# Performance work log

Hardware: AMD Instinct MI355X
Metric: run time of the kernel (lower is better)

Reference implementation:

```python
import jax, jax.numpy as jnp
import numpy as np

C, H, W = 8, 8, 8
A = 6            # action_dim
LATENT = 64
HID = 64
GRU_IN = HID + A + LATENT  # 134


def _conv(x, w):
    return jax.lax.conv_general_dilated(
        x, w, (1, 1), 'VALID', dimension_numbers=('NCHW', 'OIHW', 'NCHW'))


def setup_inputs() -> dict:
    key = jax.random.key(0)
    ks = jax.random.split(key, 20)
    B, N, T = 64, 10, 128
    s_h = jax.random.normal(ks[0], (B, N, T, C, H, W), jnp.float32)
    a_h = jax.random.randint(ks[1], (B, N, T), 0, A).astype(jnp.int64)
    b_z = jax.random.normal(ks[2], (B, LATENT), jnp.float32)
    s = 0.05
    p = {
        'conv1_w': jax.random.normal(ks[3], (32, C, 3, 3)) * s,
        'conv1_b': jnp.zeros((32,)),
        'conv2_w': jax.random.normal(ks[4], (32, 32, 3, 3)) * s,
        'conv2_b': jnp.zeros((32,)),
        'fc_w': jax.random.normal(ks[5], (HID, 32 * 4 * 4)) * s,
        'fc_b': jnp.zeros((HID,)),
        'emb': jax.random.normal(ks[6], (A, A)) * s,
        'gru_wih': jax.random.normal(ks[7], (3 * HID, GRU_IN)) * s,
        'gru_whh': jax.random.normal(ks[8], (3 * HID, HID)) * s,
        'gru_bih': jnp.zeros((3 * HID,)),
        'gru_bhh': jnp.zeros((3 * HID,)),
        'mlp1_w': jax.random.normal(ks[9], (HID, HID)) * s,
        'mlp1_b': jnp.zeros((HID,)),
        'mlp2_w': jax.random.normal(ks[10], (A, HID)) * s,
        'mlp2_b': jnp.zeros((A,)),
    }
    return {'s_h': s_h, 'a_h': a_h, 'b_z': b_z, **p}


def reference(s_h, a_h, b_z, conv1_w, conv1_b, conv2_w, conv2_b, fc_w, fc_b,
              emb, gru_wih, gru_whh, gru_bih, gru_bhh,
              mlp1_w, mlp1_b, mlp2_w, mlp2_b):
    B, N = s_h.shape[0], s_h.shape[1]
    T = a_h.shape[2]
    BN = B * N

    # action mask, [B, N, T, 1]
    action_masks = (a_h != A - 1)[..., None].astype(jnp.float32)

    # --- state encoder on first frame only ---
    s0 = s_h[:, :, 0].reshape(BN, C, H, W)
    x = jax.nn.relu(_conv(s0, conv1_w) + conv1_b[:, None, None])
    x = jax.nn.relu(_conv(x, conv2_w) + conv2_b[:, None, None])
    x = x.reshape(BN, -1)                       # [BN, 512]
    state_emb = jax.nn.relu(x @ fc_w.T + fc_b)  # [BN, HID]

    bz = jnp.broadcast_to(b_z[:, None, :], (B, N, LATENT)).reshape(BN, LATENT)

    h0 = jnp.zeros((BN, HID), s_h.dtype)
    act0 = jnp.full((BN,), A - 1, jnp.int32)

    def step(carry, _):
        h, act = carry
        a_emb = emb[act]                                          # [BN, A]
        inp = jnp.concatenate([state_emb, a_emb, bz], axis=-1)    # [BN, GRU_IN]
        gx = inp @ gru_wih.T + gru_bih
        gh = h @ gru_whh.T + gru_bhh
        xr, xz, xn = jnp.split(gx, 3, axis=-1)
        hr, hz, hn = jnp.split(gh, 3, axis=-1)
        r = jax.nn.sigmoid(xr + hr)
        z = jax.nn.sigmoid(xz + hz)
        n = jnp.tanh(xn + r * hn)
        h_new = (1.0 - z) * n + z * h
        hid = jnp.tanh(h_new @ mlp1_w.T + mlp1_b)
        logits = hid @ mlp2_w.T + mlp2_b                          # [BN, A]
        next_act = jax.lax.stop_gradient(jnp.argmax(logits, axis=-1)).astype(jnp.int32)
        return (h_new, next_act), logits

    (_, _), logits_seq = jax.lax.scan(step, (h0, act0), None, length=T - 1)
    # logits_seq: [T-1, BN, A] -> [B, N, T-1, A]
    logits_all = jnp.transpose(logits_seq, (1, 0, 2)).reshape(B, N, T - 1, A)
    return logits_all, action_masks
```

## Files before the change

kernel.cpp:

```cpp
#include <hip/hip_runtime.h>

#define A_DIM 6
#define HID_D 64
#define LATENT_D 64
#define GRU_IN_D 134
#define T_STEPS 128
#define N_ENV 10
#define BN_TOT 640

typedef float f2 __attribute__((ext_vector_type(2)));

__device__ __forceinline__ float sig_pre(float x) {
    return __builtin_amdgcn_rcpf(1.0f + __builtin_amdgcn_exp2f(x));
}
__device__ __forceinline__ float tanh_pre(float y) {
    return fmaf(-2.0f, __builtin_amdgcn_rcpf(1.0f + __builtin_amdgcn_exp2f(y)), 1.0f);
}
#define KSIG (-1.4426950408889634f)
#define KTANH (2.8853900817779268f)

template<int CTRL>
__device__ __forceinline__ float dppadd(float v) {
    int t = __builtin_amdgcn_update_dpp(0, __builtin_bit_cast(int, v), CTRL, 0xf, 0xf, true);
    return v + __builtin_bit_cast(float, t);
}
__device__ __forceinline__ float wave_reduce_add(float v) {
    v = dppadd<0x111>(v);
    v = dppadd<0x112>(v);
    v = dppadd<0x114>(v);
    v = dppadd<0x118>(v);
    v = dppadd<0x142>(v);
    v = dppadd<0x143>(v);
    return __builtin_bit_cast(float, __builtin_amdgcn_readlane(__builtin_bit_cast(int, v), 63));
}

__global__ __launch_bounds__(64) __attribute__((amdgpu_waves_per_eu(1, 1)))
void policy_kernel(const float* __restrict__ s_h,
                   const int*   __restrict__ a_h,
                   const float* __restrict__ b_z,
                   const float* __restrict__ conv1_w, const float* __restrict__ conv1_b,
                   const float* __restrict__ conv2_w, const float* __restrict__ conv2_b,
                   const float* __restrict__ fc_w,    const float* __restrict__ fc_b,
                   const float* __restrict__ emb,
                   const float* __restrict__ gru_wih, const float* __restrict__ gru_whh,
                   const float* __restrict__ gru_bih, const float* __restrict__ gru_bhh,
                   const float* __restrict__ mlp1_w,  const float* __restrict__ mlp1_b,
                   const float* __restrict__ mlp2_w,  const float* __restrict__ mlp2_b,
                   float* __restrict__ logits_out, float* __restrict__ mask_out)
{
    __shared__ __align__(16) float s0[512];
    __shared__ __align__(16) float a1[1152];
    __shared__ __align__(16) float a2[512];
    __shared__ __align__(16) float semb[64];
    __shared__ __align__(16) float gxc[192];
    __shared__ __align__(16) float hspec[6*64];

    const int bn  = blockIdx.x;
    const int tid = threadIdx.x;
    const int j   = tid;

    #pragma unroll
    for (int i = 0; i < 2; ++i) {
        const int t = tid + i * 64;
        mask_out[bn * T_STEPS + t] = (a_h[bn * T_STEPS + t] != (A_DIM - 1)) ? 1.0f : 0.0f;
    }

    {
        const float* src = s_h + (size_t)bn * T_STEPS * 512;
        #pragma unroll
        for (int i = 0; i < 8; ++i) s0[tid + i * 64] = src[tid + i * 64];
    }
    __syncthreads();

    for (int i = tid; i < 1152; i += 64) {
        const int oc = i / 36, r = i % 36, oh = r / 6, ow = r % 6;
        float sum = conv1_b[oc];
        const float* wp = conv1_w + oc * 72;
        #pragma unroll
        for (int ic = 0; ic < 8; ++ic)
            #pragma unroll
            for (int kh = 0; kh < 3; ++kh)
                #pragma unroll
                for (int kw = 0; kw < 3; ++kw)
                    sum = fmaf(s0[ic * 64 + (oh + kh) * 8 + (ow + kw)],
                               wp[ic * 9 + kh * 3 + kw], sum);
        a1[i] = fmaxf(sum, 0.0f);
    }
    __syncthreads();

    for (int i = tid; i < 512; i += 64) {
        const int oc = i / 16, r = i % 16, oh = r / 4, ow = r % 4;
        float sum = conv2_b[oc];
        const float* wp = conv2_w + oc * 288;
        for (int ic = 0; ic < 32; ++ic)
            #pragma unroll
            for (int kh = 0; kh < 3; ++kh)
                #pragma unroll
                for (int kw = 0; kw < 3; ++kw)
                    sum = fmaf(a1[ic * 36 + (oh + kh) * 6 + (ow + kw)],
                               wp[ic * 9 + kh * 3 + kw], sum);
        a2[i] = fmaxf(sum, 0.0f);
    }
    __syncthreads();

    {
        const float* wp = fc_w + j * 512;
        float s0a = 0.f, s1a = 0.f, s2a = 0.f, s3a = 0.f;
        for (int k = 0; k < 512; k += 4) {
            s0a = fmaf(a2[k + 0], wp[k + 0], s0a);
            s1a = fmaf(a2[k + 1], wp[k + 1], s1a);
            s2a = fmaf(a2[k + 2], wp[k + 2], s2a);
            s3a = fmaf(a2[k + 3], wp[k + 3], s3a);
        }
        semb[j] = fmaxf((s0a + s1a) + (s2a + s3a) + fc_b[j], 0.0f);
    }
    __syncthreads();

    {
        const float* bz = b_z + (size_t)(bn / N_ENV) * LATENT_D;
        for (int g = tid; g < 192; g += 64) {
            float sum = gru_bih[g] + ((g < 128) ? gru_bhh[g] : 0.0f);
            const float* wp = gru_wih + g * GRU_IN_D;
            for (int k = 0; k < 64; ++k) sum = fmaf(semb[k], wp[k], sum);
            for (int k = 0; k < 64; ++k) sum = fmaf(bz[k], wp[70 + k], sum);
            gxc[g] = sum;
        }
    }
    __syncthreads();

    f2 wr[32], wz[32], wn[32], w1[32];
    {
        const float* pr = gru_whh + (size_t)j * 64;
        const float* pz = gru_whh + (size_t)(64 + j) * 64;
        const float* pn = gru_whh + (size_t)(128 + j) * 64;
        const float* p1 = mlp1_w + (size_t)j * 64;
        #pragma unroll
        for (int i = 0; i < 16; ++i) {
            float4 v;
            v = ((const float4*)pr)[i];
            wr[2*i] = (f2){KSIG*v.x, KSIG*v.y}; wr[2*i+1] = (f2){KSIG*v.z, KSIG*v.w};
            v = ((const float4*)pz)[i];
            wz[2*i] = (f2){KSIG*v.x, KSIG*v.y}; wz[2*i+1] = (f2){KSIG*v.z, KSIG*v.w};
            v = ((const float4*)pn)[i];
            wn[2*i] = (f2){KTANH*v.x, KTANH*v.y}; wn[2*i+1] = (f2){KTANH*v.z, KTANH*v.w};
            v = ((const float4*)p1)[i];
            w1[2*i] = (f2){KTANH*v.x, KTANH*v.y}; w1[2*i+1] = (f2){KTANH*v.z, KTANH*v.w};
        }
    }
    const float bhn_s = KTANH * gru_bhh[128 + j];
    const float b1s   = KTANH * mlp1_b[j];

    float arx[6], azx[6], anx[6], m2c[6], b2[6];
    {
        float wqr[6], wqz[6], wqn[6];
        #pragma unroll
        for (int q = 0; q < 6; ++q) {
            wqr[q] = gru_wih[j * GRU_IN_D + 64 + q];
            wqz[q] = gru_wih[(64 + j) * GRU_IN_D + 64 + q];
            wqn[q] = gru_wih[(128 + j) * GRU_IN_D + 64 + q];
        }
        const float gxr = gxc[j], gxz = gxc[64 + j], gxn = gxc[128 + j];
        #pragma unroll
        for (int a = 0; a < 6; ++a) {
            float sr = 0.f, sz = 0.f, sn = 0.f;
            #pragma unroll
            for (int q = 0; q < 6; ++q) {
                const float e = emb[a * 6 + q];
                sr = fmaf(e, wqr[q], sr);
                sz = fmaf(e, wqz[q], sz);
                sn = fmaf(e, wqn[q], sn);
            }
            arx[a] = KSIG * (gxr + sr);
            azx[a] = KSIG * (gxz + sz);
            anx[a] = KTANH * (gxn + sn);
            m2c[a] = mlp2_w[a * 64 + j];
            b2[a] = mlp2_b[a];
        }
    }

    float ha[6];
    #pragma unroll
    for (int a = 0; a < 6; ++a) {
        const float r = sig_pre(arx[a]);
        const float z = sig_pre(azx[a]);
        const float n = tanh_pre(fmaf(r, bhn_s, anx[a]));
        ha[a] = fmaf(z, 0.0f - n, n);
    }
    __builtin_amdgcn_wave_barrier();
    #pragma unroll
    for (int a = 0; a < 6; ++a) hspec[a * 64 + j] = ha[a];
    __builtin_amdgcn_wave_barrier();

    int act = A_DIM - 1;
    float* lout = logits_out + (size_t)bn * (T_STEPS - 1) * A_DIM;

    #pragma unroll 1
    for (int t = 0; t < T_STEPS - 1; ++t) {
        const float4* hb = (const float4*)(hspec + (act << 6));
        float hprev = ha[0];
        #pragma unroll
        for (int a = 1; a < 6; ++a) hprev = (act == a) ? ha[a] : hprev;

        f2 p1a = {0.f, 0.f}, p1b = {0.f, 0.f};
        f2 pr = {0.f, 0.f}, pz = {0.f, 0.f}, pn = {0.f, 0.f};
        #pragma unroll
        for (int i = 0; i < 16; ++i) {
            const float4 hv = hb[i];
            const f2 haa = (f2){hv.x, hv.y};
            const f2 hcc = (f2){hv.z, hv.w};
            p1a += haa * w1[2*i]; p1b += hcc * w1[2*i+1];
            pr += haa * wr[2*i]; pr += hcc * wr[2*i+1];
            pz += haa * wz[2*i]; pz += hcc * wz[2*i+1];
            pn += haa * wn[2*i]; pn += hcc * wn[2*i+1];
        }
        const f2 p1 = p1a + p1b;
        const float hid = tanh_pre(p1.x + p1.y + b1s);
        const float hr = pr.x + pr.y;
        const float hz = pz.x + pz.y;
        const float hn = pn.x + pn.y + bhn_s;

        const float l0 = wave_reduce_add(hid * m2c[0]) + b2[0];
        const float l1 = wave_reduce_add(hid * m2c[1]) + b2[1];
        const float l2 = wave_reduce_add(hid * m2c[2]) + b2[2];
        const float l3 = wave_reduce_add(hid * m2c[3]) + b2[3];
        const float l4 = wave_reduce_add(hid * m2c[4]) + b2[4];
        const float l5 = wave_reduce_add(hid * m2c[5]) + b2[5];

        #pragma unroll
        for (int a = 0; a < 6; ++a) {
            const float r = sig_pre(arx[a] + hr);
            const float z = sig_pre(azx[a] + hz);
            const float n = tanh_pre(fmaf(r, hn, anx[a]));
            ha[a] = fmaf(z, hprev - n, n);
        }
        __builtin_amdgcn_wave_barrier();
        #pragma unroll
        for (int a = 0; a < 6; ++a) hspec[a * 64 + j] = ha[a];
        __builtin_amdgcn_wave_barrier();

        float best = l0; int bi = 0;
        if (l1 > best) { best = l1; bi = 1; }
        if (l2 > best) { best = l2; bi = 2; }
        if (l3 > best) { best = l3; bi = 3; }
        if (l4 > best) { best = l4; bi = 4; }
        if (l5 > best) { best = l5; bi = 5; }
        act = bi;

        if (j < A_DIM) {
            const float outv = (j == 0) ? l0 : (j == 1) ? l1 : (j == 2) ? l2
                             : (j == 3) ? l3 : (j == 4) ? l4 : l5;
            lout[t * A_DIM + j] = outv;
        }
    }
}

extern "C" void kernel_launch(void* const* d_in, const int* in_sizes, int n_in,
                              void* d_out, int out_size, void* d_ws, size_t ws_size,
                              hipStream_t stream) {
    const float* s_h     = (const float*)d_in[0];
    const int*   a_h     = (const int*)  d_in[1];
    const float* b_z     = (const float*)d_in[2];
    const float* conv1_w = (const float*)d_in[3];
    const float* conv1_b = (const float*)d_in[4];
    const float* conv2_w = (const float*)d_in[5];
    const float* conv2_b = (const float*)d_in[6];
    const float* fc_w    = (const float*)d_in[7];
    const float* fc_b    = (const float*)d_in[8];
    const float* emb     = (const float*)d_in[9];
    const float* gru_wih = (const float*)d_in[10];
    const float* gru_whh = (const float*)d_in[11];
    const float* gru_bih = (const float*)d_in[12];
    const float* gru_bhh = (const float*)d_in[13];
    const float* mlp1_w  = (const float*)d_in[14];
    const float* mlp1_b  = (const float*)d_in[15];
    const float* mlp2_w  = (const float*)d_in[16];
    const float* mlp2_b  = (const float*)d_in[17];

    float* out = (float*)d_out;
    float* logits_out = out;
    float* mask_out   = out + (size_t)BN_TOT * (T_STEPS - 1) * A_DIM;

    policy_kernel<<<BN_TOT, 64, 0, stream>>>(
        s_h, a_h, b_z, conv1_w, conv1_b, conv2_w, conv2_b, fc_w, fc_b, emb,
        gru_wih, gru_whh, gru_bih, gru_bhh, mlp1_w, mlp1_b, mlp2_w, mlp2_b,
        logits_out, mask_out);
}
```

Baseline: 513.6 us.

## Split GRU recurrence across four waves per block with LDS exchange

Grows each block from one wave to four. Each wave now owns one of the r/z/n/mlp1 weight matrices in registers, and the waves exchange partial results through LDS with two block barriers per timestep. The conv, fc and input-projection prologue is also spread over 256 threads, and logits are staged in LDS and written out once at the end. This cuts the per-wave serial FMA work and register pressure in the recurrent loop, at the cost of __syncthreads latency on the 127-step critical path.

```diff
diff --git a/kernel.cpp b/kernel.cpp
--- a/kernel.cpp
+++ b/kernel.cpp
@@ -10,14 +10,14 @@
 
 typedef float f2 __attribute__((ext_vector_type(2)));
 
+#define KSIG (-1.4426950408889634f)
+#define KTANH (2.8853900817779268f)
 __device__ __forceinline__ float sig_pre(float x) {
     return __builtin_amdgcn_rcpf(1.0f + __builtin_amdgcn_exp2f(x));
 }
 __device__ __forceinline__ float tanh_pre(float y) {
     return fmaf(-2.0f, __builtin_amdgcn_rcpf(1.0f + __builtin_amdgcn_exp2f(y)), 1.0f);
 }
-#define KSIG (-1.4426950408889634f)
-#define KTANH (2.8853900817779268f)
 
 template<int CTRL>
 __device__ __forceinline__ float dppadd(float v) {
@@ -34,7 +34,7 @@
     return __builtin_bit_cast(float, __builtin_amdgcn_readlane(__builtin_bit_cast(int, v), 63));
 }
 
-__global__ __launch_bounds__(64) __attribute__((amdgpu_waves_per_eu(1, 1)))
+__global__ __launch_bounds__(256)
 void policy_kernel(const float* __restrict__ s_h,
                    const int*   __restrict__ a_h,
                    const float* __restrict__ b_z,
@@ -49,30 +49,32 @@
                    float* __restrict__ logits_out, float* __restrict__ mask_out)
 {
     __shared__ __align__(16) float s0[512];
-    __shared__ __align__(16) float a1[1152];
-    __shared__ __align__(16) float a2[512];
+    __shared__ __align__(16) float a1s[1152];
+    __shared__ __align__(16) float a2s[512];
+    __shared__ __align__(16) float pfc[256];
     __shared__ __align__(16) float semb[64];
     __shared__ __align__(16) float gxc[192];
     __shared__ __align__(16) float hspec[6*64];
+    __shared__ __align__(16) float hrzn[3*64];
+    __shared__ __align__(16) float llog[(T_STEPS-1)*A_DIM];
+    __shared__ int act_lds;
 
     const int bn  = blockIdx.x;
     const int tid = threadIdx.x;
-    const int j   = tid;
-
-    #pragma unroll
-    for (int i = 0; i < 2; ++i) {
-        const int t = tid + i * 64;
-        mask_out[bn * T_STEPS + t] = (a_h[bn * T_STEPS + t] != (A_DIM - 1)) ? 1.0f : 0.0f;
-    }
+    const int j   = tid & 63;
+    const int w   = tid >> 6;
+
+    if (tid < 128)
+        mask_out[bn * T_STEPS + tid] = (a_h[bn * T_STEPS + tid] != (A_DIM - 1)) ? 1.0f : 0.0f;
 
     {
         const float* src = s_h + (size_t)bn * T_STEPS * 512;
-        #pragma unroll
-        for (int i = 0; i < 8; ++i) s0[tid + i * 64] = src[tid + i * 64];
-    }
-    __syncthreads();
-
-    for (int i = tid; i < 1152; i += 64) {
+        s0[tid]       = src[tid];
+        s0[tid + 256] = src[tid + 256];
+    }
+    __syncthreads();
+
+    for (int i = tid; i < 1152; i += 256) {
         const int oc = i / 36, r = i % 36, oh = r / 6, ow = r % 6;
         float sum = conv1_b[oc];
         const float* wp = conv1_w + oc * 72;
@@ -84,11 +86,11 @@
                 for (int kw = 0; kw < 3; ++kw)
                     sum = fmaf(s0[ic * 64 + (oh + kh) * 8 + (ow + kw)],
                                wp[ic * 9 + kh * 3 + kw], sum);
-        a1[i] = fmaxf(sum, 0.0f);
-    }
-    __syncthreads();
-
-    for (int i = tid; i < 512; i += 64) {
+        a1s[i] = fmaxf(sum, 0.0f);
+    }
+    __syncthreads();
+
+    for (int i = tid; i < 512; i += 256) {
         const int oc = i / 16, r = i % 16, oh = r / 4, ow = r % 4;
         float sum = conv2_b[oc];
         const float* wp = conv2_w + oc * 288;
@@ -97,61 +99,63 @@
             for (int kh = 0; kh < 3; ++kh)
                 #pragma unroll
                 for (int kw = 0; kw < 3; ++kw)
-                    sum = fmaf(a1[ic * 36 + (oh + kh) * 6 + (ow + kw)],
+                    sum = fmaf(a1s[ic * 36 + (oh + kh) * 6 + (ow + kw)],
                                wp[ic * 9 + kh * 3 + kw], sum);
-        a2[i] = fmaxf(sum, 0.0f);
-    }
-    __syncthreads();
-
-    {
-        const float* wp = fc_w + j * 512;
+        a2s[i] = fmaxf(sum, 0.0f);
+    }
+    __syncthreads();
+
+    {
+        const float* wp = fc_w + j * 512 + w * 128;
+        const float* ap = a2s + w * 128;
         float s0a = 0.f, s1a = 0.f, s2a = 0.f, s3a = 0.f;
-        for (int k = 0; k < 512; k += 4) {
-            s0a = fmaf(a2[k + 0], wp[k + 0], s0a);
-            s1a = fmaf(a2[k + 1], wp[k + 1], s1a);
-            s2a = fmaf(a2[k + 2], wp[k + 2], s2a);
-            s3a = fmaf(a2[k + 3], wp[k + 3], s3a);
-        }
-        semb[j] = fmaxf((s0a + s1a) + (s2a + s3a) + fc_b[j], 0.0f);
-    }
-    __syncthreads();
-
-    {
+        for (int k = 0; k < 128; k += 4) {
+            s0a = fmaf(ap[k + 0], wp[k + 0], s0a);
+            s1a = fmaf(ap[k + 1], wp[k + 1], s1a);
+            s2a = fmaf(ap[k + 2], wp[k + 2], s2a);
+            s3a = fmaf(ap[k + 3], wp[k + 3], s3a);
+        }
+        pfc[tid] = (s0a + s1a) + (s2a + s3a);
+    }
+    __syncthreads();
+    if (tid < 64)
+        semb[tid] = fmaxf(pfc[tid] + pfc[tid + 64] + pfc[tid + 128] + pfc[tid + 192]
+                          + fc_b[tid], 0.0f);
+    __syncthreads();
+
+    if (tid < 192) {
         const float* bz = b_z + (size_t)(bn / N_ENV) * LATENT_D;
-        for (int g = tid; g < 192; g += 64) {
-            float sum = gru_bih[g] + ((g < 128) ? gru_bhh[g] : 0.0f);
-            const float* wp = gru_wih + g * GRU_IN_D;
-            for (int k = 0; k < 64; ++k) sum = fmaf(semb[k], wp[k], sum);
-            for (int k = 0; k < 64; ++k) sum = fmaf(bz[k], wp[70 + k], sum);
-            gxc[g] = sum;
-        }
-    }
-    __syncthreads();
-
-    f2 wr[32], wz[32], wn[32], w1[32];
-    {
-        const float* pr = gru_whh + (size_t)j * 64;
-        const float* pz = gru_whh + (size_t)(64 + j) * 64;
-        const float* pn = gru_whh + (size_t)(128 + j) * 64;
-        const float* p1 = mlp1_w + (size_t)j * 64;
+        const int g = tid;
+        float sum = gru_bih[g] + ((g < 128) ? gru_bhh[g] : 0.0f);
+        const float* wp = gru_wih + g * GRU_IN_D;
+        for (int k = 0; k < 64; ++k) sum = fmaf(semb[k], wp[k], sum);
+        for (int k = 0; k < 64; ++k) sum = fmaf(bz[k], wp[70 + k], sum);
+        gxc[g] = sum;
+    }
+    __syncthreads();
+
+    f2 wm[32];
+    {
+        const float* src = (w == 0) ? gru_whh + (size_t)j * 64
+                         : (w == 1) ? gru_whh + (size_t)(64 + j) * 64
+                         : (w == 2) ? gru_whh + (size_t)(128 + j) * 64
+                         :            mlp1_w  + (size_t)j * 64;
+        const float ks = (w < 2) ? KSIG : KTANH;
         #pragma unroll
         for (int i = 0; i < 16; ++i) {
-            float4 v;
-            v = ((const float4*)pr)[i];
-            wr[2*i] = (f2){KSIG*v.x, KSIG*v.y}; wr[2*i+1] = (f2){KSIG*v.z, KSIG*v.w};
-            v = ((const float4*)pz)[i];
-            wz[2*i] = (f2){KSIG*v.x, KSIG*v.y}; wz[2*i+1] = (f2){KSIG*v.z, KSIG*v.w};
-            v = ((const float4*)pn)[i];
-            wn[2*i] = (f2){KTANH*v.x, KTANH*v.y}; wn[2*i+1] = (f2){KTANH*v.z, KTANH*v.w};
-            v = ((const float4*)p1)[i];
-            w1[2*i] = (f2){KTANH*v.x, KTANH*v.y}; w1[2*i+1] = (f2){KTANH*v.z, KTANH*v.w};
+            const float4 v = ((const float4*)src)[i];
+            wm[2*i]   = (f2){ks * v.x, ks * v.y};
+            wm[2*i+1] = (f2){ks * v.z, ks * v.w};
         }
     }
     const float bhn_s = KTANH * gru_bhh[128 + j];
-    const float b1s   = KTANH * mlp1_b[j];
-
-    float arx[6], azx[6], anx[6], m2c[6], b2[6];
-    {
+
+    float arx0 = 0.f, azx0 = 0.f, anx0 = 0.f;
+    float arx1 = 0.f, azx1 = 0.f, anx1 = 0.f;
+    float m2c[6], b2v[6];
+    float b1s = 0.f;
+
+    if (w < 3) {
         float wqr[6], wqz[6], wqn[6];
         #pragma unroll
         for (int q = 0; q < 6; ++q) {
@@ -161,7 +165,8 @@
         }
         const float gxr = gxc[j], gxz = gxc[64 + j], gxn = gxc[128 + j];
         #pragma unroll
-        for (int a = 0; a < 6; ++a) {
+        for (int s = 0; s < 2; ++s) {
+            const int a = 2 * w + s;
             float sr = 0.f, sz = 0.f, sn = 0.f;
             #pragma unroll
             for (int q = 0; q < 6; ++q) {
@@ -170,87 +175,88 @@
                 sz = fmaf(e, wqz[q], sz);
                 sn = fmaf(e, wqn[q], sn);
             }
-            arx[a] = KSIG * (gxr + sr);
-            azx[a] = KSIG * (gxz + sz);
-            anx[a] = KTANH * (gxn + sn);
-            m2c[a] = mlp2_w[a * 64 + j];
-            b2[a] = mlp2_b[a];
-        }
-    }
-
-    float ha[6];
-    #pragma unroll
-    for (int a = 0; a < 6; ++a) {
-        const float r = sig_pre(arx[a]);
-        const float z = sig_pre(azx[a]);
-        const float n = tanh_pre(fmaf(r, bhn_s, anx[a]));
-        ha[a] = fmaf(z, 0.0f - n, n);
-    }
-    __builtin_amdgcn_wave_barrier();
-    #pragma unroll
-    for (int a = 0; a < 6; ++a) hspec[a * 64 + j] = ha[a];
-    __builtin_amdgcn_wave_barrier();
-
-    int act = A_DIM - 1;
-    float* lout = logits_out + (size_t)bn * (T_STEPS - 1) * A_DIM;
-
-    #pragma unroll 1
+            if (s == 0) { arx0 = KSIG*(gxr+sr); azx0 = KSIG*(gxz+sz); anx0 = KTANH*(gxn+sn); }
+            else        { arx1 = KSIG*(gxr+sr); azx1 = KSIG*(gxz+sz); anx1 = KTANH*(gxn+sn); }
+        }
+        {
+            float r = sig_pre(arx0);
+            float z = sig_pre(azx0);
+            float n = tanh_pre(fmaf(r, bhn_s, anx0));
+            hspec[(2*w) * 64 + j] = fmaf(z, 0.0f - n, n);
+            r = sig_pre(arx1);
+            z = sig_pre(azx1);
+            n = tanh_pre(fmaf(r, bhn_s, anx1));
+            hspec[(2*w+1) * 64 + j] = fmaf(z, 0.0f - n, n);
+        }
+    } else {
+        #pragma unroll
+        for (int a = 0; a < 6; ++a) { m2c[a] = mlp2_w[a * 64 + j]; b2v[a] = mlp2_b[a]; }
+        b1s = KTANH * mlp1_b[j];
+    }
+    if (tid == 0) act_lds = A_DIM - 1;
+    __syncthreads();
+
     for (int t = 0; t < T_STEPS - 1; ++t) {
+        const int act = act_lds;
         const float4* hb = (const float4*)(hspec + (act << 6));
-        float hprev = ha[0];
-        #pragma unroll
-        for (int a = 1; a < 6; ++a) hprev = (act == a) ? ha[a] : hprev;
-
-        f2 p1a = {0.f, 0.f}, p1b = {0.f, 0.f};
-        f2 pr = {0.f, 0.f}, pz = {0.f, 0.f}, pn = {0.f, 0.f};
-        #pragma unroll
-        for (int i = 0; i < 16; ++i) {
-            const float4 hv = hb[i];
-            const f2 haa = (f2){hv.x, hv.y};
-            const f2 hcc = (f2){hv.z, hv.w};
-            p1a += haa * w1[2*i]; p1b += hcc * w1[2*i+1];
-            pr += haa * wr[2*i]; pr += hcc * wr[2*i+1];
-            pz += haa * wz[2*i]; pz += hcc * wz[2*i+1];
-            pn += haa * wn[2*i]; pn += hcc * wn[2*i+1];
-        }
-        const f2 p1 = p1a + p1b;
-        const float hid = tanh_pre(p1.x + p1.y + b1s);
-        const float hr = pr.x + pr.y;
-        const float hz = pz.x + pz.y;
-        const float hn = pn.x + pn.y + bhn_s;
-
-        const float l0 = wave_reduce_add(hid * m2c[0]) + b2[0];
-        const float l1 = wave_reduce_add(hid * m2c[1]) + b2[1];
-        const float l2 = wave_reduce_add(hid * m2c[2]) + b2[2];
-        const float l3 = wave_reduce_add(hid * m2c[3]) + b2[3];
-        const float l4 = wave_reduce_add(hid * m2c[4]) + b2[4];
-        const float l5 = wave_reduce_add(hid * m2c[5]) + b2[5];
-
-        #pragma unroll
-        for (int a = 0; a < 6; ++a) {
-            const float r = sig_pre(arx[a] + hr);
-            const float z = sig_pre(azx[a] + hz);
-            const float n = tanh_pre(fmaf(r, hn, anx[a]));
-            ha[a] = fmaf(z, hprev - n, n);
-        }
-        __builtin_amdgcn_wave_barrier();
-        #pragma unroll
-        for (int a = 0; a < 6; ++a) hspec[a * 64 + j] = ha[a];
-        __builtin_amdgcn_wave_barrier();
-
-        float best = l0; int bi = 0;
-        if (l1 > best) { best = l1; bi = 1; }
-        if (l2 > best) { best = l2; bi = 2; }
-        if (l3 > best) { best = l3; bi = 3; }
-        if (l4 > best) { best = l4; bi = 4; }
-        if (l5 > best) { best = l5; bi = 5; }
-        act = bi;
-
-        if (j < A_DIM) {
-            const float outv = (j == 0) ? l0 : (j == 1) ? l1 : (j == 2) ? l2
-                             : (j == 3) ? l3 : (j == 4) ? l4 : l5;
-            lout[t * A_DIM + j] = outv;
-        }
+        const float hprev = hspec[(act << 6) + j];
+
+        f2 q0 = {0.f,0.f}, q1 = {0.f,0.f}, q2 = {0.f,0.f}, q3 = {0.f,0.f};
+        #pragma unroll
+        for (int i = 0; i < 8; ++i) {
+            const float4 u = hb[i];
+            const float4 v = hb[i + 8];
+            q0 += (f2){u.x, u.y} * wm[2*i];
+            q1 += (f2){u.z, u.w} * wm[2*i+1];
+            q2 += (f2){v.x, v.y} * wm[2*i+16];
+            q3 += (f2){v.z, v.w} * wm[2*i+17];
+        }
+        const f2 qs = (q0 + q1) + (q2 + q3);
+        float sres = qs.x + qs.y;
+
+        float hid = 0.0f;
+        if (w == 2) sres += bhn_s;
+        if (w < 3)  hrzn[w * 64 + j] = sres;
+        else        hid = tanh_pre(sres + b1s);
+        __syncthreads();
+
+        if (w < 3) {
+            const float hr = hrzn[j], hz = hrzn[64 + j], hn = hrzn[128 + j];
+            float r = sig_pre(arx0 + hr);
+            float z = sig_pre(azx0 + hz);
+            float n = tanh_pre(fmaf(r, hn, anx0));
+            hspec[(2*w) * 64 + j] = fmaf(z, hprev - n, n);
+            r = sig_pre(arx1 + hr);
+            z = sig_pre(azx1 + hz);
+            n = tanh_pre(fmaf(r, hn, anx1));
+            hspec[(2*w+1) * 64 + j] = fmaf(z, hprev - n, n);
+        } else {
+            const float l0 = wave_reduce_add(hid * m2c[0]) + b2v[0];
+            const float l1 = wave_reduce_add(hid * m2c[1]) + b2v[1];
+            const float l2 = wave_reduce_add(hid * m2c[2]) + b2v[2];
+            const float l3 = wave_reduce_add(hid * m2c[3]) + b2v[3];
+            const float l4 = wave_reduce_add(hid * m2c[4]) + b2v[4];
+            const float l5 = wave_reduce_add(hid * m2c[5]) + b2v[5];
+
+            if (j < A_DIM) {
+                const float outv = (j == 0) ? l0 : (j == 1) ? l1 : (j == 2) ? l2
+                                 : (j == 3) ? l3 : (j == 4) ? l4 : l5;
+                llog[t * A_DIM + j] = outv;
+            }
+            float best = l0; int bi = 0;
+            if (l1 > best) { best = l1; bi = 1; }
+            if (l2 > best) { best = l2; bi = 2; }
+            if (l3 > best) { best = l3; bi = 3; }
+            if (l4 > best) { best = l4; bi = 4; }
+            if (l5 > best) { best = l5; bi = 5; }
+            if (j == 0) act_lds = bi;
+        }
+        __syncthreads();
+    }
+
+    {
+        float* lout = logits_out + (size_t)bn * (T_STEPS - 1) * A_DIM;
+        for (int i = tid; i < (T_STEPS - 1) * A_DIM; i += 256) lout[i] = llog[i];
     }
 }
 
@@ -280,7 +286,7 @@
     float* logits_out = out;
     float* mask_out   = out + (size_t)BN_TOT * (T_STEPS - 1) * A_DIM;
 
-    policy_kernel<<<BN_TOT, 64, 0, stream>>>(
+    policy_kernel<<<BN_TOT, 256, 0, stream>>>(
         s_h, a_h, b_z, conv1_w, conv1_b, conv2_w, conv2_b, fc_w, fc_b, emb,
         gru_wih, gru_whh, gru_bih, gru_bhh, mlp1_w, mlp1_b, mlp2_w, mlp2_b,
         logits_out, mask_out);
```

Result: slower. 532.0 us (+3.6%).
